# Kernel tuning notes

Hardware: AMD Instinct MI355X
Metric: run time of the kernel (lower is better)

Reference implementation:

```python
import jax, jax.numpy as jnp
import numpy as np

F = 64      # input_v_size
E = 64      # emb_v_size
H = 8       # int(sqrt(emb_v_size))
P = 512     # proj_e_size
B, T = 64, 256


def setup_inputs() -> dict:
    key = jax.random.key(0)
    ks = jax.random.split(key, 14)
    s1 = 1.0            # Linear(1->H): fan_in=1
    s2 = 1.0 / np.sqrt(H)
    s3 = 1.0 / np.sqrt(F * E)
    return {
        "x":    jax.random.normal(ks[0], (B, T, F), dtype=jnp.float32),
        "time": jax.random.uniform(ks[1], (B, T, F), dtype=jnp.float32),
        # stacked per-feature Linear(1->H): weight [F,H], bias [F,H]
        "w1v": jax.random.uniform(ks[2], (F, H), jnp.float32, -s1, s1),
        "b1v": jax.random.uniform(ks[3], (F, H), jnp.float32, -s1, s1),
        # stacked per-feature Linear(H->E, bias=False): [F,H,E]
        "w2v": jax.random.uniform(ks[4], (F, H, E), jnp.float32, -s2, s2),
        "w1t": jax.random.uniform(ks[5], (F, H), jnp.float32, -s1, s1),
        "b1t": jax.random.uniform(ks[6], (F, H), jnp.float32, -s1, s1),
        "w2t": jax.random.uniform(ks[7], (F, H, E), jnp.float32, -s2, s2),
        # Wx, Wt: Linear(F*E -> P) stored as [F*E, P] (= torch weight.T)
        "wx":  jax.random.uniform(ks[8], (F * E, P), jnp.float32, -s3, s3),
        "bx":  jax.random.uniform(ks[9], (P,), jnp.float32, -s3, s3),
        "wt":  jax.random.uniform(ks[10], (F * E, P), jnp.float32, -s3, s3),
        "bt":  jax.random.uniform(ks[11], (P,), jnp.float32, -s3, s3),
    }


def _branch(inp, w1, b1, w2):
    # inp [B,T,F]; w1,b1 [F,H]; w2 [F,H,E]
    h = jnp.tanh(inp[..., None] * w1 + b1)          # [B,T,F,H]
    e = jnp.einsum("btfh,fhe->btfe", h, w2)          # [B,T,F,E]
    return e.reshape(*inp.shape[:2], -1)              # [B,T,F*E]


def reference(x, time, w1v, b1v, w2v, w1t, b1t, w2t, wx, bx, wt, bt):
    x_out = _branch(x, w1v, b1v, w2v)
    t_out = _branch(time, w1t, b1t, w2t)
    return (x_out @ wx + bx) + (t_out @ wt + bt)      # [B,T,P]
```

## Files before the change

kernel.cpp:

```cpp
#include <hip/hip_runtime.h>
#include <cstdint>
#include <cstddef>

#define FF 64
#define EE 64
#define HH 8
#define PP 512
#define MM 16384
#define KK 1024

typedef __bf16 bf16x8 __attribute__((ext_vector_type(8)));
typedef float  floatx4 __attribute__((ext_vector_type(4)));

__device__ __forceinline__ unsigned short f2bf(float f) {
    unsigned int u = __float_as_uint(f);
    u += 0x7FFFu + ((u >> 16) & 1u);
    return (unsigned short)(u >> 16);
}

__device__ __forceinline__ unsigned pack2(unsigned short a, unsigned short b) {
    return (unsigned)a | ((unsigned)b << 16);
}

__device__ __forceinline__ float fast_tanh_s(float t) {
    float e, r;
    asm("v_exp_f32 %0, %1" : "=v"(e) : "v"(t));
    float d = e + 1.0f;
    asm("v_rcp_f32 %0, %1" : "=v"(r) : "v"(d));
    return __builtin_fmaf(-2.0f, r, 1.0f);
}

__global__ __launch_bounds__(256) void combine_kernel(
    const float* __restrict__ w2v, const float* __restrict__ w2t,
    const float* __restrict__ wx,  const float* __restrict__ wt,
    unsigned short* __restrict__ BmatT)
{
    const int tid = threadIdx.x;
    const int bid = blockIdx.x;
    const int br = bid >> 7;
    const int f  = (bid >> 1) & 63;
    const int nh = bid & 1;
    const float* __restrict__ w2 = br ? w2t : w2v;
    const float* __restrict__ W  = br ? wt  : wx;
    __shared__ float w2s[HH * EE];
    for (int i = tid; i < HH * EE; i += 256) w2s[i] = w2[f * HH * EE + i];
    __syncthreads();
    const int n = nh * 256 + tid;
    float acc[HH] = {0,0,0,0,0,0,0,0};
    const float* Wcol = W + (size_t)f * EE * PP + n;
    #pragma unroll 8
    for (int e = 0; e < EE; ++e) {
        const float wv = Wcol[(size_t)e * PP];
        #pragma unroll
        for (int h = 0; h < HH; ++h)
            acc[h] = __builtin_fmaf(w2s[h * EE + e], wv, acc[h]);
    }
    uint4 v;
    v.x = pack2(f2bf(acc[0]), f2bf(acc[1]));
    v.y = pack2(f2bf(acc[2]), f2bf(acc[3]));
    v.z = pack2(f2bf(acc[4]), f2bf(acc[5]));
    v.w = pack2(f2bf(acc[6]), f2bf(acc[7]));
    *reinterpret_cast<uint4*>(&BmatT[(size_t)n * KK + br * 512 + f * 8]) = v;
}

__global__ __launch_bounds__(256, 2) void gemm_fused_kernel(
    const float* __restrict__ x,   const float* __restrict__ tmv,
    const float* __restrict__ w1v, const float* __restrict__ b1v,
    const float* __restrict__ w1t, const float* __restrict__ b1t,
    const unsigned short* __restrict__ Bt,
    const float* __restrict__ bx, const float* __restrict__ bt,
    float* __restrict__ out)
{
    __shared__ __align__(16) unsigned short As[64 * 64];
    __shared__ __align__(16) float w1s[2 * FF * HH];
    __shared__ __align__(16) float b1s[2 * FF * HH];

    const int tid  = threadIdx.x;
    const int wave = tid >> 6;
    const int lane = tid & 63;
    const int m0 = blockIdx.x * 64;
    const int n0 = blockIdx.y * 256;

    {
        const float c = 2.8853900817779268f;
        const float4 wsrc = (tid < 128) ? reinterpret_cast<const float4*>(w1v)[tid]
                                        : reinterpret_cast<const float4*>(w1t)[tid - 128];
        const float4 bsrc = (tid < 128) ? reinterpret_cast<const float4*>(b1v)[tid]
                                        : reinterpret_cast<const float4*>(b1t)[tid - 128];
        float4 ws, bs;
        ws.x = wsrc.x * c; ws.y = wsrc.y * c; ws.z = wsrc.z * c; ws.w = wsrc.w * c;
        bs.x = bsrc.x * c; bs.y = bsrc.y * c; bs.z = bsrc.z * c; bs.w = bsrc.w * c;
        reinterpret_cast<float4*>(w1s)[tid] = ws;
        reinterpret_cast<float4*>(b1s)[tid] = bs;
    }

    const int wn  = wave;
    const int q   = lane >> 4;
    const int ml  = lane & 15;
    const int mlx = ml & 7;
    const int fi  = tid & 7;
    const int g   = tid >> 3;
    const int pchunkA = (fi ^ (g & 7)) * 8;

    const unsigned short* BtL = Bt + (size_t)(n0 + wn * 64 + ml) * KK + q * 8;

    __syncthreads();

    float4 wlo, whi, blo, bhi;
    float  va, vb;
    uint4  pa, pb;

    wlo = reinterpret_cast<const float4*>(w1s)[fi * 2];
    whi = reinterpret_cast<const float4*>(w1s)[fi * 2 + 1];
    blo = reinterpret_cast<const float4*>(b1s)[fi * 2];
    bhi = reinterpret_cast<const float4*>(b1s)[fi * 2 + 1];
    va = x[(size_t)(m0 + g) * FF + fi];
    vb = x[(size_t)(m0 + g + 32) * FF + fi];

    auto tanh_pack = [&](float val) -> uint4 {
        float hv[8];
        hv[0] = fast_tanh_s(__builtin_fmaf(val, wlo.x, blo.x));
        hv[1] = fast_tanh_s(__builtin_fmaf(val, wlo.y, blo.y));
        hv[2] = fast_tanh_s(__builtin_fmaf(val, wlo.z, blo.z));
        hv[3] = fast_tanh_s(__builtin_fmaf(val, wlo.w, blo.w));
        hv[4] = fast_tanh_s(__builtin_fmaf(val, whi.x, bhi.x));
        hv[5] = fast_tanh_s(__builtin_fmaf(val, whi.y, bhi.y));
        hv[6] = fast_tanh_s(__builtin_fmaf(val, whi.z, bhi.z));
        hv[7] = fast_tanh_s(__builtin_fmaf(val, whi.w, bhi.w));
        uint4 v;
        v.x = pack2(f2bf(hv[0]), f2bf(hv[1]));
        v.y = pack2(f2bf(hv[2]), f2bf(hv[3]));
        v.z = pack2(f2bf(hv[4]), f2bf(hv[5]));
        v.w = pack2(f2bf(hv[6]), f2bf(hv[7]));
        return v;
    };
    pa = tanh_pack(va);
    pb = tanh_pack(vb);

    floatx4 acc[4][4];
    #pragma unroll
    for (int i = 0; i < 4; ++i)
        #pragma unroll
        for (int j = 0; j < 4; ++j)
            acc[i][j] = (floatx4){0.f, 0.f, 0.f, 0.f};

    for (int it = 0; it < 16; ++it) {
        const int k0 = it * 64;

        *reinterpret_cast<uint4*>(&As[g * 64 + pchunkA])        = pa;
        *reinterpret_cast<uint4*>(&As[(g + 32) * 64 + pchunkA]) = pb;
        __syncthreads();

        const int itn = (it < 15) ? it + 1 : 15;
        const int brn = itn >> 3;
        const int fn  = ((itn & 7) << 3) + fi;
        const float* __restrict__ inpn = brn ? tmv : x;
        const float nva = inpn[(size_t)(m0 + g) * FF + fn];
        const float nvb = inpn[(size_t)(m0 + g + 32) * FF + fn];
        const float4 nwlo = reinterpret_cast<const float4*>(w1s)[brn * 128 + fn * 2];
        const float4 nwhi = reinterpret_cast<const float4*>(w1s)[brn * 128 + fn * 2 + 1];
        const float4 nblo = reinterpret_cast<const float4*>(b1s)[brn * 128 + fn * 2];
        const float4 nbhi = reinterpret_cast<const float4*>(b1s)[brn * 128 + fn * 2 + 1];

        bf16x8 bfr0[4], bfr1[4];
        #pragma unroll
        for (int nt = 0; nt < 4; ++nt)
            bfr0[nt] = *reinterpret_cast<const bf16x8*>(&BtL[(size_t)nt * 16 * KK + k0]);
        #pragma unroll
        for (int nt = 0; nt < 4; ++nt)
            bfr1[nt] = *reinterpret_cast<const bf16x8*>(&BtL[(size_t)nt * 16 * KK + k0 + 32]);

        {
            const int co0 = ((0 + q) ^ mlx) * 8;
            bf16x8 af[4];
            #pragma unroll
            for (int mt = 0; mt < 4; ++mt)
                af[mt] = *reinterpret_cast<const bf16x8*>(&As[(mt * 16 + ml) * 64 + co0]);
            #pragma unroll
            for (int mt = 0; mt < 4; ++mt)
                #pragma unroll
                for (int nt = 0; nt < 4; ++nt)
                    acc[mt][nt] = __builtin_amdgcn_mfma_f32_16x16x32_bf16(
                        af[mt], bfr0[nt], acc[mt][nt], 0, 0, 0);

            wlo = nwlo; whi = nwhi; blo = nblo; bhi = nbhi;
            va = nva; vb = nvb;
            pa = tanh_pack(va);
            pb = tanh_pack(vb);

            const int co1 = ((4 + q) ^ mlx) * 8;
            #pragma unroll
            for (int mt = 0; mt < 4; ++mt)
                af[mt] = *reinterpret_cast<const bf16x8*>(&As[(mt * 16 + ml) * 64 + co1]);
            #pragma unroll
            for (int mt = 0; mt < 4; ++mt)
                #pragma unroll
                for (int nt = 0; nt < 4; ++nt)
                    acc[mt][nt] = __builtin_amdgcn_mfma_f32_16x16x32_bf16(
                        af[mt], bfr1[nt], acc[mt][nt], 0, 0, 0);
        }
        __syncthreads();
    }

    float bias[4];
    #pragma unroll
    for (int nt = 0; nt < 4; ++nt) {
        const int n = n0 + wn * 64 + nt * 16 + ml;
        bias[nt] = bx[n] + bt[n];
    }
    #pragma unroll
    for (int mt = 0; mt < 4; ++mt) {
        const int mb = m0 + mt * 16 + q * 4;
        #pragma unroll
        for (int r = 0; r < 4; ++r) {
            float* orow = out + (size_t)(mb + r) * PP + n0 + wn * 64 + ml;
            #pragma unroll
            for (int nt = 0; nt < 4; ++nt)
                orow[nt * 16] = acc[mt][nt][r] + bias[nt];
        }
    }
}

extern "C" void kernel_launch(void* const* d_in, const int* in_sizes, int n_in,
                              void* d_out, int out_size, void* d_ws, size_t ws_size,
                              hipStream_t stream)
{
    const float* x   = (const float*)d_in[0];
    const float* tmv = (const float*)d_in[1];
    const float* w1v = (const float*)d_in[2];
    const float* b1v = (const float*)d_in[3];
    const float* w2v = (const float*)d_in[4];
    const float* w1t = (const float*)d_in[5];
    const float* b1t = (const float*)d_in[6];
    const float* w2t = (const float*)d_in[7];
    const float* wx  = (const float*)d_in[8];
    const float* bx  = (const float*)d_in[9];
    const float* wt  = (const float*)d_in[10];
    const float* bt  = (const float*)d_in[11];
    float* out = (float*)d_out;

    unsigned short* Bws = (unsigned short*)d_ws;

    combine_kernel<<<256, 256, 0, stream>>>(w2v, w2t, wx, wt, Bws);
    gemm_fused_kernel<<<dim3(MM / 64, PP / 256), 256, 0, stream>>>(
        x, tmv, w1v, b1v, w1t, b1t, Bws, bx, bt, out);
}
```

Before: 145.2 us.

## Double-buffer A tile in LDS and prefetch next B fragments across iterations

Doubles the LDS A tile so each iteration writes the tanh-generated next tile into the other buffer while MFMAs read the current one. This cuts the two block barriers per K step down to one. B fragments for the next step are loaded from global memory one iteration ahead into a second register set, hiding their latency behind the current MFMAs. In exchange it uses more LDS and more VGPRs for the extra fragment set, which may reduce occupancy under launch_bounds(256,2). The hand-written s_waitcnt/s_barrier asm does not wait on vmcnt, so correctness depends on the compiler inserting the right waits for the global loads.

After: 135.2 us. 1.07x faster.

```diff
diff --git a/kernel.cpp b/kernel.cpp
--- a/kernel.cpp
+++ b/kernel.cpp
@@ -71,7 +71,7 @@
     const float* __restrict__ bx, const float* __restrict__ bt,
     float* __restrict__ out)
 {
-    __shared__ __align__(16) unsigned short As[64 * 64];
+    __shared__ __align__(16) unsigned short As[2][64 * 64];
     __shared__ __align__(16) float w1s[2 * FF * HH];
     __shared__ __align__(16) float b1s[2 * FF * HH];
 
@@ -104,18 +104,9 @@
 
     const unsigned short* BtL = Bt + (size_t)(n0 + wn * 64 + ml) * KK + q * 8;
 
-    __syncthreads();
-
     float4 wlo, whi, blo, bhi;
     float  va, vb;
     uint4  pa, pb;
-
-    wlo = reinterpret_cast<const float4*>(w1s)[fi * 2];
-    whi = reinterpret_cast<const float4*>(w1s)[fi * 2 + 1];
-    blo = reinterpret_cast<const float4*>(b1s)[fi * 2];
-    bhi = reinterpret_cast<const float4*>(b1s)[fi * 2 + 1];
-    va = x[(size_t)(m0 + g) * FF + fi];
-    vb = x[(size_t)(m0 + g + 32) * FF + fi];
 
     auto tanh_pack = [&](float val) -> uint4 {
         float hv[8];
@@ -134,8 +125,25 @@
         v.w = pack2(f2bf(hv[6]), f2bf(hv[7]));
         return v;
     };
+
+    va = x[(size_t)(m0 + g) * FF + fi];
+    vb = x[(size_t)(m0 + g + 32) * FF + fi];
+    bf16x8 bfrC[8], bfrN[8];
+    #pragma unroll
+    for (int nt = 0; nt < 4; ++nt) {
+        bfrC[nt * 2]     = *reinterpret_cast<const bf16x8*>(&BtL[(size_t)nt * 16 * KK]);
+        bfrC[nt * 2 + 1] = *reinterpret_cast<const bf16x8*>(&BtL[(size_t)nt * 16 * KK + 32]);
+    }
+    __syncthreads();
+    wlo = reinterpret_cast<const float4*>(w1s)[fi * 2];
+    whi = reinterpret_cast<const float4*>(w1s)[fi * 2 + 1];
+    blo = reinterpret_cast<const float4*>(b1s)[fi * 2];
+    bhi = reinterpret_cast<const float4*>(b1s)[fi * 2 + 1];
     pa = tanh_pack(va);
     pb = tanh_pack(vb);
+    *reinterpret_cast<uint4*>(&As[0][g * 64 + pchunkA])        = pa;
+    *reinterpret_cast<uint4*>(&As[0][(g + 32) * 64 + pchunkA]) = pb;
+    asm volatile("s_waitcnt lgkmcnt(0)\n\ts_barrier" ::: "memory");
 
     floatx4 acc[4][4];
     #pragma unroll
@@ -145,61 +153,66 @@
             acc[i][j] = (floatx4){0.f, 0.f, 0.f, 0.f};
 
     for (int it = 0; it < 16; ++it) {
-        const int k0 = it * 64;
-
-        *reinterpret_cast<uint4*>(&As[g * 64 + pchunkA])        = pa;
-        *reinterpret_cast<uint4*>(&As[(g + 32) * 64 + pchunkA]) = pb;
-        __syncthreads();
-
+        const int buf = it & 1;
         const int itn = (it < 15) ? it + 1 : 15;
         const int brn = itn >> 3;
         const int fn  = ((itn & 7) << 3) + fi;
+
         const float* __restrict__ inpn = brn ? tmv : x;
         const float nva = inpn[(size_t)(m0 + g) * FF + fn];
         const float nvb = inpn[(size_t)(m0 + g + 32) * FF + fn];
+
+        {
+            const unsigned short* src = BtL + (size_t)itn * 64;
+            #pragma unroll
+            for (int nt = 0; nt < 4; ++nt) {
+                bfrN[nt * 2]     = *reinterpret_cast<const bf16x8*>(&src[(size_t)nt * 16 * KK]);
+                bfrN[nt * 2 + 1] = *reinterpret_cast<const bf16x8*>(&src[(size_t)nt * 16 * KK + 32]);
+            }
+        }
+
         const float4 nwlo = reinterpret_cast<const float4*>(w1s)[brn * 128 + fn * 2];
         const float4 nwhi = reinterpret_cast<const float4*>(w1s)[brn * 128 + fn * 2 + 1];
         const float4 nblo = reinterpret_cast<const float4*>(b1s)[brn * 128 + fn * 2];
         const float4 nbhi = reinterpret_cast<const float4*>(b1s)[brn * 128 + fn * 2 + 1];
 
-        bf16x8 bfr0[4], bfr1[4];
-        #pragma unroll
-        for (int nt = 0; nt < 4; ++nt)
-            bfr0[nt] = *reinterpret_cast<const bf16x8*>(&BtL[(size_t)nt * 16 * KK + k0]);
-        #pragma unroll
-        for (int nt = 0; nt < 4; ++nt)
-            bfr1[nt] = *reinterpret_cast<const bf16x8*>(&BtL[(size_t)nt * 16 * KK + k0 + 32]);
-
+        bf16x8 af[4];
         {
             const int co0 = ((0 + q) ^ mlx) * 8;
-            bf16x8 af[4];
-            #pragma unroll
-            for (int mt = 0; mt < 4; ++mt)
-                af[mt] = *reinterpret_cast<const bf16x8*>(&As[(mt * 16 + ml) * 64 + co0]);
+            #pragma unroll
+            for (int mt = 0; mt < 4; ++mt)
+                af[mt] = *reinterpret_cast<const bf16x8*>(&As[buf][(mt * 16 + ml) * 64 + co0]);
             #pragma unroll
             for (int mt = 0; mt < 4; ++mt)
                 #pragma unroll
                 for (int nt = 0; nt < 4; ++nt)
                     acc[mt][nt] = __builtin_amdgcn_mfma_f32_16x16x32_bf16(
-                        af[mt], bfr0[nt], acc[mt][nt], 0, 0, 0);
-
-            wlo = nwlo; whi = nwhi; blo = nblo; bhi = nbhi;
-            va = nva; vb = nvb;
-            pa = tanh_pack(va);
-            pb = tanh_pack(vb);
-
+                        af[mt], bfrC[nt * 2], acc[mt][nt], 0, 0, 0);
+        }
+
+        wlo = nwlo; whi = nwhi; blo = nblo; bhi = nbhi;
+        pa = tanh_pack(nva);
+        pb = tanh_pack(nvb);
+        *reinterpret_cast<uint4*>(&As[buf ^ 1][g * 64 + pchunkA])        = pa;
+        *reinterpret_cast<uint4*>(&As[buf ^ 1][(g + 32) * 64 + pchunkA]) = pb;
+
+        {
             const int co1 = ((4 + q) ^ mlx) * 8;
             #pragma unroll
             for (int mt = 0; mt < 4; ++mt)
-                af[mt] = *reinterpret_cast<const bf16x8*>(&As[(mt * 16 + ml) * 64 + co1]);
+                af[mt] = *reinterpret_cast<const bf16x8*>(&As[buf][(mt * 16 + ml) * 64 + co1]);
             #pragma unroll
             for (int mt = 0; mt < 4; ++mt)
                 #pragma unroll
                 for (int nt = 0; nt < 4; ++nt)
                     acc[mt][nt] = __builtin_amdgcn_mfma_f32_16x16x32_bf16(
-                        af[mt], bfr1[nt], acc[mt][nt], 0, 0, 0);
-        }
-        __syncthreads();
+                        af[mt], bfrC[nt * 2 + 1], acc[mt][nt], 0, 0, 0);
+        }
+
+        asm volatile("s_waitcnt lgkmcnt(0)\n\ts_barrier" ::: "memory");
+
+        #pragma unroll
+        for (int i = 0; i < 8; ++i) bfrC[i] = bfrN[i];
     }
 
     float bias[4];
```
